# Performance work log

Measured on AMD Instinct MI355X. Metric: run time of the kernel, lower is better.

Reference implementation:

```python
import jax, jax.numpy as jnp
import numpy as np

N_NODES = 50000
N_EDGES = 800000
D_IN = 128
HIDDEN = 64
N_CLASSES = 2


def gcn_conv(x, edge_index, W, b, num_nodes):
    """PyG GCNConv: linear (no bias) -> add self-loops -> sym-normalized aggregate -> + bias."""
    h = x @ W  # [N, H]
    loop = jnp.arange(num_nodes, dtype=edge_index.dtype)
    src = jnp.concatenate([edge_index[0], loop])  # [E+N]
    dst = jnp.concatenate([edge_index[1], loop])
    deg = jax.ops.segment_sum(jnp.ones_like(dst, dtype=h.dtype), dst, num_segments=num_nodes)
    dinv = jnp.where(deg > 0, jax.lax.rsqrt(deg), 0.0)
    norm = dinv[src] * dinv[dst]  # [E+N]
    msg = h[src] * norm[:, None]  # [E+N, H]  (gather + scale)
    out = jax.ops.segment_sum(msg, dst, num_segments=num_nodes)  # scatter-add
    return out + b


def setup_inputs() -> dict:
    key = jax.random.key(0)
    ks = jax.random.split(key, 6)
    x = jax.random.normal(ks[0], (N_NODES, D_IN), dtype=jnp.float32)
    edge_index = jax.random.randint(ks[1], (2, N_EDGES), 0, N_NODES, dtype=jnp.int64)
    # Glorot-ish init for weights, zero bias (PyG default)
    W1 = jax.random.normal(ks[2], (D_IN, HIDDEN), dtype=jnp.float32) * (1.0 / np.sqrt(D_IN))
    b1 = jnp.zeros((HIDDEN,), dtype=jnp.float32)
    W2 = jax.random.normal(ks[3], (HIDDEN, N_CLASSES), dtype=jnp.float32) * (1.0 / np.sqrt(HIDDEN))
    b2 = jnp.zeros((N_CLASSES,), dtype=jnp.float32)
    return {"x": x, "edge_index": edge_index, "W1": W1, "b1": b1, "W2": W2, "b2": b2}


def reference(x, edge_index, W1, b1, W2, b2):
    h = jax.nn.relu(gcn_conv(x, edge_index, W1, b1, N_NODES))
    # F.dropout(training=self.training) is identity in eval mode
    out = gcn_conv(h, edge_index, W2, b2, N_NODES)
    return out
```

## Files before the change

### kernel.cpp

```cpp
#include <hip/hip_runtime.h>

#define N_NODES 50000
#define N_EDGES 800000
#define D_IN 128
#define HIDDEN 64
#define N_CLASSES 2
#define NBUK 782
#define NBUK_P 784
#define NBLK 196
#define NE4 200000
#define XPAD 136
#define CAP 2048

typedef _Float16 half4v __attribute__((ext_vector_type(4)));
typedef _Float16 h8 __attribute__((ext_vector_type(8)));
typedef float f4 __attribute__((ext_vector_type(4)));
typedef float f8 __attribute__((ext_vector_type(8)));


__global__ __launch_bounds__(256) void k_gemm_bin(
    const int4* __restrict__ src4, const int4* __restrict__ dst4,
    int* __restrict__ cnt, int* __restrict__ ebin,
    const float* __restrict__ x, const float* __restrict__ W1,
    _Float16* __restrict__ hs)
{
    __shared__ __attribute__((aligned(16))) _Float16 smem[2 * 64 * XPAD];
    const int t = threadIdx.x;

    if (blockIdx.x < NBLK) {
        int* hist = (int*)smem;
        int* curb = (int*)smem + NBUK_P;
        for (int i = t; i < NBUK; i += 256) hist[i] = 0;
        __syncthreads();
        int base4 = blockIdx.x * 1024;
#pragma unroll
        for (int k = 0; k < 4; k++) {
            int idx = base4 + k * 256 + t;
            if (idx < NE4) {
                int4 d = dst4[idx];
                atomicAdd(&hist[d.x >> 6], 1);
                atomicAdd(&hist[d.y >> 6], 1);
                atomicAdd(&hist[d.z >> 6], 1);
                atomicAdd(&hist[d.w >> 6], 1);
            }
        }
        __syncthreads();
        for (int i = t; i < NBUK; i += 256) {
            int c = hist[i];
            curb[i] = c ? atomicAdd(&cnt[i], c) : 0;
        }
        __syncthreads();
#pragma unroll
        for (int k = 0; k < 4; k++) {
            int idx = base4 + k * 256 + t;
            if (idx < NE4) {
                int4 sv = src4[idx];
                int4 d = dst4[idx];
                int p0 = atomicAdd(&curb[d.x >> 6], 1);
                int p1 = atomicAdd(&curb[d.y >> 6], 1);
                int p2 = atomicAdd(&curb[d.z >> 6], 1);
                int p3 = atomicAdd(&curb[d.w >> 6], 1);
                if (p0 < CAP) ebin[(d.x >> 6) * CAP + p0] = (sv.x << 7) | (d.x & 63);
                if (p1 < CAP) ebin[(d.y >> 6) * CAP + p1] = (sv.y << 7) | (d.y & 63);
                if (p2 < CAP) ebin[(d.z >> 6) * CAP + p2] = (sv.z << 7) | (d.z & 63);
                if (p3 < CAP) ebin[(d.w >> 6) * CAP + p3] = (sv.w << 7) | (d.w & 63);
            }
        }
        return;
    }

    _Float16* xs = smem;
    _Float16* Wt = smem + 64 * XPAD;
    const int gb = blockIdx.x - NBLK;
    const int row0 = gb * 64;

    for (int i4 = t; i4 < 64 * D_IN / 4; i4 += 256) {
        int r = i4 >> 5;
        int k4 = (i4 & 31) << 2;
        int grow = row0 + r;
        half4v hv;
        if (grow < N_NODES) {
            float4 v = *(const float4*)&x[grow * D_IN + k4];
            hv.x = (_Float16)v.x; hv.y = (_Float16)v.y;
            hv.z = (_Float16)v.z; hv.w = (_Float16)v.w;
        } else {
            hv.x = hv.y = hv.z = hv.w = (_Float16)0.f;
        }
        *(half4v*)&xs[r * XPAD + k4] = hv;
    }
    for (int i4 = t; i4 < D_IN * HIDDEN / 4; i4 += 256) {
        float4 v = *(const float4*)&W1[i4 * 4];
        int k = i4 >> 4;
        int n = (i4 & 15) << 2;
        Wt[(n + 0) * XPAD + k] = (_Float16)v.x;
        Wt[(n + 1) * XPAD + k] = (_Float16)v.y;
        Wt[(n + 2) * XPAD + k] = (_Float16)v.z;
        Wt[(n + 3) * XPAD + k] = (_Float16)v.w;
    }
    __syncthreads();

    const int w = t >> 6;
    const int L = t & 63;
    const int mrow = w * 16 + (L & 15);
    const int qk = (L >> 4) * 8;
    f4 acc0 = {0.f, 0.f, 0.f, 0.f}, acc1 = acc0, acc2 = acc0, acc3 = acc0;
#pragma unroll
    for (int ks = 0; ks < D_IN; ks += 32) {
        h8 a  = *(const h8*)&xs[mrow * XPAD + ks + qk];
        h8 b0 = *(const h8*)&Wt[(0 * 16 + (L & 15)) * XPAD + ks + qk];
        h8 b1 = *(const h8*)&Wt[(1 * 16 + (L & 15)) * XPAD + ks + qk];
        h8 b2 = *(const h8*)&Wt[(2 * 16 + (L & 15)) * XPAD + ks + qk];
        h8 b3 = *(const h8*)&Wt[(3 * 16 + (L & 15)) * XPAD + ks + qk];
        acc0 = __builtin_amdgcn_mfma_f32_16x16x32_f16(a, b0, acc0, 0, 0, 0);
        acc1 = __builtin_amdgcn_mfma_f32_16x16x32_f16(a, b1, acc1, 0, 0, 0);
        acc2 = __builtin_amdgcn_mfma_f32_16x16x32_f16(a, b2, acc2, 0, 0, 0);
        acc3 = __builtin_amdgcn_mfma_f32_16x16x32_f16(a, b3, acc3, 0, 0, 0);
    }

    const int n0 = L & 15;
#pragma unroll
    for (int j = 0; j < 4; j++) {
        int m = w * 16 + (L >> 4) * 4 + j;
        size_t base = (size_t)(row0 + m) * HIDDEN;
        hs[base + 0 * 16 + n0] = (_Float16)acc0[j];
        hs[base + 1 * 16 + n0] = (_Float16)acc1[j];
        hs[base + 2 * 16 + n0] = (_Float16)acc2[j];
        hs[base + 3 * 16 + n0] = (_Float16)acc3[j];
    }
}


__global__ __launch_bounds__(256) void k_csr_scale(
    const int* __restrict__ ebin, const int* __restrict__ cnt,
    int* __restrict__ rs, int* __restrict__ re, float* __restrict__ dinv_g,
    int* __restrict__ rec, _Float16* __restrict__ hs)
{
    __shared__ int cnt64[64];
    __shared__ int cur[64];
    __shared__ float sdinv[64];
    const int b = blockIdx.x;
    const int t = threadIdx.x;
    const int row0 = b * 64;
    const int beg = b * CAP;
    const int end = beg + cnt[b];

    if (t < 64) cnt64[t] = 0;
    __syncthreads();
    for (int i = beg + t; i < end; i += 256) atomicAdd(&cnt64[ebin[i] & 63], 1);
    __syncthreads();
    if (t < 64) {
        int deg = cnt64[t];
        int sum = deg;
#pragma unroll
        for (int off = 1; off < 64; off <<= 1) {
            int v = __shfl_up(sum, off, 64);
            if (t >= off) sum += v;
        }
        int ex = sum - deg;
        cur[t] = ex;
        float di = rsqrtf((float)(deg + 1));
        sdinv[t] = di;
        int node = row0 + t;
        rs[node] = beg + ex;
        re[node] = beg + ex + deg;
        dinv_g[node] = di;
    }
    __syncthreads();
    for (int i = beg + t; i < end; i += 256) {
        int pk = ebin[i];
        int pos = atomicAdd(&cur[pk & 63], 1);
        rec[beg + pos] = pk >> 7;
    }
    for (int i = t; i < 64 * HIDDEN / 8; i += 256) {
        int r = i >> 3;
        int c = (i & 7) << 3;
        size_t base = (size_t)(row0 + r) * HIDDEN + c;
        h8 hv = *(const h8*)&hs[base];
        float di = sdinv[r];
#pragma unroll
        for (int k = 0; k < 8; k++) hv[k] = (_Float16)((float)hv[k] * di);
        *(h8*)&hs[base] = hv;
    }
}


__global__ __launch_bounds__(256) void k_agg1_l2(
    const _Float16* __restrict__ hs, const int* __restrict__ rs,
    const int* __restrict__ re,
    const int* __restrict__ rec, const float* __restrict__ dinv,
    const float* __restrict__ b1, const float* __restrict__ W2,
    float* __restrict__ zs)
{
    const int node = blockIdx.x * 32 + (threadIdx.x >> 3);
    const int g = threadIdx.x & 7;
    const int gbase = threadIdx.x & 56;
    const h8* H = (const h8*)hs;

    float di = dinv[node];
    f8 acc = {};

    int beg = rs[node];
    int end = re[node];

    for (int base = beg; base < end; base += 16) {
        int n = end - base;
        if (n > 16) n = 16;
        int r0 = (2 * g     < n) ? rec[base + 2 * g]     : N_NODES;
        int r1 = (2 * g + 1 < n) ? rec[base + 2 * g + 1] : N_NODES;
        int n8 = (n + 7) & ~7;
        for (int e = 0; e < n8; e += 8) {
            int q = gbase + (e >> 1);
            int s0 = __shfl(r0, q + 0, 64);
            int s1 = __shfl(r1, q + 0, 64);
            int s2 = __shfl(r0, q + 1, 64);
            int s3 = __shfl(r1, q + 1, 64);
            int s4 = __shfl(r0, q + 2, 64);
            int s5 = __shfl(r1, q + 2, 64);
            int s6 = __shfl(r0, q + 3, 64);
            int s7 = __shfl(r1, q + 3, 64);
            h8 a0 = H[s0 * 8 + g];
            h8 a1 = H[s1 * 8 + g];
            h8 a2 = H[s2 * 8 + g];
            h8 a3 = H[s3 * 8 + g];
            h8 a4 = H[s4 * 8 + g];
            h8 a5 = H[s5 * 8 + g];
            h8 a6 = H[s6 * 8 + g];
            h8 a7 = H[s7 * 8 + g];
#pragma unroll
            for (int k = 0; k < 8; k++) {
                acc[k] += (((float)a0[k] + (float)a1[k]) + ((float)a2[k] + (float)a3[k]))
                        + (((float)a4[k] + (float)a5[k]) + ((float)a6[k] + (float)a7[k]));
            }
        }
    }

    h8 sv = H[node * 8 + g];
#pragma unroll
    for (int k = 0; k < 8; k++) acc[k] += (float)sv[k];

    float4 bbA = ((const float4*)b1)[2 * g];
    float4 bbB = ((const float4*)b1)[2 * g + 1];
    float y[8];
    y[0] = fmaxf(fmaf(acc[0], di, bbA.x), 0.f);
    y[1] = fmaxf(fmaf(acc[1], di, bbA.y), 0.f);
    y[2] = fmaxf(fmaf(acc[2], di, bbA.z), 0.f);
    y[3] = fmaxf(fmaf(acc[3], di, bbA.w), 0.f);
    y[4] = fmaxf(fmaf(acc[4], di, bbB.x), 0.f);
    y[5] = fmaxf(fmaf(acc[5], di, bbB.y), 0.f);
    y[6] = fmaxf(fmaf(acc[6], di, bbB.z), 0.f);
    y[7] = fmaxf(fmaf(acc[7], di, bbB.w), 0.f);
    float p0 = 0.f, p1 = 0.f;
    const float4* W2f4 = (const float4*)W2;
#pragma unroll
    for (int m = 0; m < 4; m++) {
        float4 q = W2f4[4 * g + m];
        p0 += y[2 * m] * q.x + y[2 * m + 1] * q.z;
        p1 += y[2 * m] * q.y + y[2 * m + 1] * q.w;
    }

    p0 += __shfl_down(p0, 4, 64);
    p1 += __shfl_down(p1, 4, 64);
    p0 += __shfl_down(p0, 2, 64);
    p1 += __shfl_down(p1, 2, 64);
    p0 += __shfl_down(p0, 1, 64);
    p1 += __shfl_down(p1, 1, 64);
    if (g == 0) {
        zs[node * 2 + 0] = p0 * di;
        zs[node * 2 + 1] = p1 * di;
    }
}


__global__ __launch_bounds__(256) void k_agg2(
    const float* __restrict__ zs, const int* __restrict__ rs,
    const int* __restrict__ re,
    const int* __restrict__ rec, const float* __restrict__ dinv,
    const float* __restrict__ b2, float* __restrict__ out)
{
    const int node = blockIdx.x * 32 + (threadIdx.x >> 3);
    const int j = threadIdx.x & 7;
    if (node >= N_NODES) return;
    int beg = rs[node];
    int end = re[node];
    float a0 = 0.f, a1 = 0.f;
    for (int idx = beg + j; idx < end; idx += 8) {
        int s = rec[idx];
        float2 v = *(const float2*)&zs[s * 2];
        a0 += v.x;
        a1 += v.y;
    }
    a0 += __shfl_down(a0, 4, 64);
    a1 += __shfl_down(a1, 4, 64);
    a0 += __shfl_down(a0, 2, 64);
    a1 += __shfl_down(a1, 2, 64);
    a0 += __shfl_down(a0, 1, 64);
    a1 += __shfl_down(a1, 1, 64);
    if (j == 0) {
        float di = dinv[node];
        float2 zv = *(const float2*)&zs[node * 2];
        float2 o;
        o.x = fmaf(di, a0 + zv.x, b2[0]);
        o.y = fmaf(di, a1 + zv.y, b2[1]);
        *(float2*)&out[node * 2] = o;
    }
}


extern "C" void kernel_launch(void* const* d_in, const int* in_sizes, int n_in,
                              void* d_out, int out_size, void* d_ws, size_t ws_size,
                              hipStream_t stream) {
    const float* x  = (const float*)d_in[0];
    const int* ei   = (const int*)d_in[1];
    const float* W1 = (const float*)d_in[2];
    const float* b1 = (const float*)d_in[3];
    const float* W2 = (const float*)d_in[4];
    const float* b2 = (const float*)d_in[5];
    float* out = (float*)d_out;

    const int4* src4 = (const int4*)ei;
    const int4* dst4 = (const int4*)(ei + N_EDGES);

    int*      cnt  = (int*)d_ws;
    float*    dinv = (float*)d_ws + 2048;
    int*      rs   = (int*)d_ws + 53248;
    int*      re   = (int*)d_ws + 104448;
    int*      ebin = (int*)d_ws + 155648;
    int*      rec  = (int*)d_ws + 1757184;
    _Float16* hs   = (_Float16*)((int*)d_ws + 3358720);
    float*    zs   = (float*)d_ws + 4960256;

    hipMemsetAsync(cnt, 0, 1024 * sizeof(int), stream);
    k_gemm_bin<<<NBLK + NBUK, 256, 0, stream>>>(src4, dst4, cnt, ebin, x, W1, hs);
    k_csr_scale<<<NBUK, 256, 0, stream>>>(ebin, cnt, rs, re, dinv, rec, hs);
    k_agg1_l2<<<(N_NODES + 31) / 32, 256, 0, stream>>>(hs, rs, re, rec, dinv, b1, W2, zs);
    k_agg2<<<(N_NODES + 31) / 32, 256, 0, stream>>>(zs, rs, re, rec, dinv, b2, out);
}
```

Measured before the change: 120.2 us.

## Prefetch edge indices in aggregation loops and cache edge bins in registers/LDS

New measurement: 122.8 us. 1.02x slower.

```diff
diff --git a/kernel.cpp b/kernel.cpp
--- a/kernel.cpp
+++ b/kernel.cpp
@@ -6,7 +6,6 @@
 #define HIDDEN 64
 #define N_CLASSES 2
 #define NBUK 782
-#define NBUK_P 784
 #define NBLK 196
 #define NE4 200000
 #define XPAD 136
@@ -29,41 +28,43 @@
 
     if (blockIdx.x < NBLK) {
         int* hist = (int*)smem;
-        int* curb = (int*)smem + NBUK_P;
         for (int i = t; i < NBUK; i += 256) hist[i] = 0;
         __syncthreads();
         int base4 = blockIdx.x * 1024;
+        int4 dv[4], sv[4];
+        bool val[4];
 #pragma unroll
         for (int k = 0; k < 4; k++) {
             int idx = base4 + k * 256 + t;
-            if (idx < NE4) {
-                int4 d = dst4[idx];
-                atomicAdd(&hist[d.x >> 6], 1);
-                atomicAdd(&hist[d.y >> 6], 1);
-                atomicAdd(&hist[d.z >> 6], 1);
-                atomicAdd(&hist[d.w >> 6], 1);
+            val[k] = (idx < NE4);
+            if (val[k]) {
+                dv[k] = dst4[idx];
+                sv[k] = src4[idx];
+                atomicAdd(&hist[dv[k].x >> 6], 1);
+                atomicAdd(&hist[dv[k].y >> 6], 1);
+                atomicAdd(&hist[dv[k].z >> 6], 1);
+                atomicAdd(&hist[dv[k].w >> 6], 1);
             }
         }
         __syncthreads();
         for (int i = t; i < NBUK; i += 256) {
             int c = hist[i];
-            curb[i] = c ? atomicAdd(&cnt[i], c) : 0;
+            hist[i] = c ? atomicAdd(&cnt[i], c) : 0;
         }
         __syncthreads();
 #pragma unroll
         for (int k = 0; k < 4; k++) {
-            int idx = base4 + k * 256 + t;
-            if (idx < NE4) {
-                int4 sv = src4[idx];
-                int4 d = dst4[idx];
-                int p0 = atomicAdd(&curb[d.x >> 6], 1);
-                int p1 = atomicAdd(&curb[d.y >> 6], 1);
-                int p2 = atomicAdd(&curb[d.z >> 6], 1);
-                int p3 = atomicAdd(&curb[d.w >> 6], 1);
-                if (p0 < CAP) ebin[(d.x >> 6) * CAP + p0] = (sv.x << 7) | (d.x & 63);
-                if (p1 < CAP) ebin[(d.y >> 6) * CAP + p1] = (sv.y << 7) | (d.y & 63);
-                if (p2 < CAP) ebin[(d.z >> 6) * CAP + p2] = (sv.z << 7) | (d.z & 63);
-                if (p3 < CAP) ebin[(d.w >> 6) * CAP + p3] = (sv.w << 7) | (d.w & 63);
+            if (val[k]) {
+                int b0 = dv[k].x >> 6, b1 = dv[k].y >> 6;
+                int b2 = dv[k].z >> 6, b3 = dv[k].w >> 6;
+                int p0 = atomicAdd(&hist[b0], 1);
+                int p1 = atomicAdd(&hist[b1], 1);
+                int p2 = atomicAdd(&hist[b2], 1);
+                int p3 = atomicAdd(&hist[b3], 1);
+                if (p0 < CAP) ebin[b0 * CAP + p0] = (sv[k].x << 7) | (dv[k].x & 63);
+                if (p1 < CAP) ebin[b1 * CAP + p1] = (sv[k].y << 7) | (dv[k].y & 63);
+                if (p2 < CAP) ebin[b2 * CAP + p2] = (sv[k].z << 7) | (dv[k].z & 63);
+                if (p3 < CAP) ebin[b3 * CAP + p3] = (sv[k].w << 7) | (dv[k].w & 63);
             }
         }
         return;
@@ -135,6 +136,7 @@
     int* __restrict__ rs, int* __restrict__ re, float* __restrict__ dinv_g,
     int* __restrict__ rec, _Float16* __restrict__ hs)
 {
+    __shared__ int lbin[CAP];
     __shared__ int cnt64[64];
     __shared__ int cur[64];
     __shared__ float sdinv[64];
@@ -142,11 +144,15 @@
     const int t = threadIdx.x;
     const int row0 = b * 64;
     const int beg = b * CAP;
-    const int end = beg + cnt[b];
+    const int m = cnt[b];
 
     if (t < 64) cnt64[t] = 0;
     __syncthreads();
-    for (int i = beg + t; i < end; i += 256) atomicAdd(&cnt64[ebin[i] & 63], 1);
+    for (int i = t; i < m; i += 256) {
+        int pk = ebin[beg + i];
+        lbin[i] = pk;
+        atomicAdd(&cnt64[pk & 63], 1);
+    }
     __syncthreads();
     if (t < 64) {
         int deg = cnt64[t];
@@ -166,8 +172,8 @@
         dinv_g[node] = di;
     }
     __syncthreads();
-    for (int i = beg + t; i < end; i += 256) {
-        int pk = ebin[i];
+    for (int i = t; i < m; i += 256) {
+        int pk = lbin[i];
         int pos = atomicAdd(&cur[pk & 63], 1);
         rec[beg + pos] = pk >> 7;
     }
@@ -202,11 +208,23 @@
     int beg = rs[node];
     int end = re[node];
 
+    int r0 = N_NODES, r1 = N_NODES;
+    if (beg < end) {
+        int n0 = end - beg; if (n0 > 16) n0 = 16;
+        if (2 * g     < n0) r0 = rec[beg + 2 * g];
+        if (2 * g + 1 < n0) r1 = rec[beg + 2 * g + 1];
+    }
+
     for (int base = beg; base < end; base += 16) {
+        int nb = base + 16;
+        int nr0 = N_NODES, nr1 = N_NODES;
+        if (nb < end) {
+            int nn = end - nb; if (nn > 16) nn = 16;
+            if (2 * g     < nn) nr0 = rec[nb + 2 * g];
+            if (2 * g + 1 < nn) nr1 = rec[nb + 2 * g + 1];
+        }
         int n = end - base;
         if (n > 16) n = 16;
-        int r0 = (2 * g     < n) ? rec[base + 2 * g]     : N_NODES;
-        int r1 = (2 * g + 1 < n) ? rec[base + 2 * g + 1] : N_NODES;
         int n8 = (n + 7) & ~7;
         for (int e = 0; e < n8; e += 8) {
             int q = gbase + (e >> 1);
@@ -232,6 +250,7 @@
                         + (((float)a4[k] + (float)a5[k]) + ((float)a6[k] + (float)a7[k]));
             }
         }
+        r0 = nr0; r1 = nr1;
     }
 
     h8 sv = H[node * 8 + g];
@@ -283,11 +302,16 @@
     int beg = rs[node];
     int end = re[node];
     float a0 = 0.f, a1 = 0.f;
-    for (int idx = beg + j; idx < end; idx += 8) {
-        int s = rec[idx];
+    int idx = beg + j;
+    int s = (idx < end) ? rec[idx] : 0;
+    while (idx < end) {
+        int nidx = idx + 8;
+        int ns = (nidx < end) ? rec[nidx] : 0;
         float2 v = *(const float2*)&zs[s * 2];
         a0 += v.x;
         a1 += v.y;
+        idx = nidx;
+        s = ns;
     }
     a0 += __shfl_down(a0, 4, 64);
     a1 += __shfl_down(a1, 4, 64);
```

## Split hidden features into two halves and aggregate each half in separate passes

Applied to the files above, without the earlier changes.

New measurement: 129.1 us. 7.4% more time.

```diff
diff --git a/kernel.cpp b/kernel.cpp
--- a/kernel.cpp
+++ b/kernel.cpp
@@ -15,14 +15,13 @@
 typedef _Float16 half4v __attribute__((ext_vector_type(4)));
 typedef _Float16 h8 __attribute__((ext_vector_type(8)));
 typedef float f4 __attribute__((ext_vector_type(4)));
-typedef float f8 __attribute__((ext_vector_type(8)));
 
 
 __global__ __launch_bounds__(256) void k_gemm_bin(
     const int4* __restrict__ src4, const int4* __restrict__ dst4,
     int* __restrict__ cnt, int* __restrict__ ebin,
     const float* __restrict__ x, const float* __restrict__ W1,
-    _Float16* __restrict__ hs)
+    _Float16* __restrict__ hs0, _Float16* __restrict__ hs1)
 {
     __shared__ __attribute__((aligned(16))) _Float16 smem[2 * 64 * XPAD];
     const int t = threadIdx.x;
@@ -121,11 +120,11 @@
 #pragma unroll
     for (int j = 0; j < 4; j++) {
         int m = w * 16 + (L >> 4) * 4 + j;
-        size_t base = (size_t)(row0 + m) * HIDDEN;
-        hs[base + 0 * 16 + n0] = (_Float16)acc0[j];
-        hs[base + 1 * 16 + n0] = (_Float16)acc1[j];
-        hs[base + 2 * 16 + n0] = (_Float16)acc2[j];
-        hs[base + 3 * 16 + n0] = (_Float16)acc3[j];
+        size_t bh = (size_t)(row0 + m) * 32;
+        hs0[bh + n0]      = (_Float16)acc0[j];
+        hs0[bh + 16 + n0] = (_Float16)acc1[j];
+        hs1[bh + n0]      = (_Float16)acc2[j];
+        hs1[bh + 16 + n0] = (_Float16)acc3[j];
     }
 }
 
@@ -133,7 +132,7 @@
 __global__ __launch_bounds__(256) void k_csr_scale(
     const int* __restrict__ ebin, const int* __restrict__ cnt,
     int* __restrict__ rs, int* __restrict__ re, float* __restrict__ dinv_g,
-    int* __restrict__ rec, _Float16* __restrict__ hs)
+    int* __restrict__ rec, _Float16* __restrict__ hs0, _Float16* __restrict__ hs1)
 {
     __shared__ int cnt64[64];
     __shared__ int cur[64];
@@ -171,33 +170,35 @@
         int pos = atomicAdd(&cur[pk & 63], 1);
         rec[beg + pos] = pk >> 7;
     }
-    for (int i = t; i < 64 * HIDDEN / 8; i += 256) {
-        int r = i >> 3;
-        int c = (i & 7) << 3;
-        size_t base = (size_t)(row0 + r) * HIDDEN + c;
-        h8 hv = *(const h8*)&hs[base];
+    for (int i = t; i < 512; i += 256) {
+        int sel = i >> 8;
+        int idx = i & 255;
+        int r = idx >> 2;
+        int c = (idx & 3) << 3;
+        _Float16* hp = sel ? hs1 : hs0;
+        size_t base = (size_t)(row0 + r) * 32 + c;
+        h8 hv = *(const h8*)&hp[base];
         float di = sdinv[r];
 #pragma unroll
         for (int k = 0; k < 8; k++) hv[k] = (_Float16)((float)hv[k] * di);
-        *(h8*)&hs[base] = hv;
-    }
-}
-
-
-__global__ __launch_bounds__(256) void k_agg1_l2(
-    const _Float16* __restrict__ hs, const int* __restrict__ rs,
-    const int* __restrict__ re,
-    const int* __restrict__ rec, const float* __restrict__ dinv,
-    const float* __restrict__ b1, const float* __restrict__ W2,
-    float* __restrict__ zs)
+        *(h8*)&hp[base] = hv;
+    }
+}
+
+
+__global__ __launch_bounds__(256) void k_agg1_half(
+    const _Float16* __restrict__ hsh, const int* __restrict__ rs,
+    const int* __restrict__ re, const int* __restrict__ rec,
+    const float* __restrict__ dinv, const float* __restrict__ b1h,
+    const float* __restrict__ W2h, float* __restrict__ zs, int accum)
 {
     const int node = blockIdx.x * 32 + (threadIdx.x >> 3);
     const int g = threadIdx.x & 7;
     const int gbase = threadIdx.x & 56;
-    const h8* H = (const h8*)hs;
+    const half4v* H = (const half4v*)hsh;
 
     float di = dinv[node];
-    f8 acc = {};
+    f4 acc = {0.f, 0.f, 0.f, 0.f};
 
     int beg = rs[node];
     int end = re[node];
@@ -218,45 +219,40 @@
             int s5 = __shfl(r1, q + 2, 64);
             int s6 = __shfl(r0, q + 3, 64);
             int s7 = __shfl(r1, q + 3, 64);
-            h8 a0 = H[s0 * 8 + g];
-            h8 a1 = H[s1 * 8 + g];
-            h8 a2 = H[s2 * 8 + g];
-            h8 a3 = H[s3 * 8 + g];
-            h8 a4 = H[s4 * 8 + g];
-            h8 a5 = H[s5 * 8 + g];
-            h8 a6 = H[s6 * 8 + g];
-            h8 a7 = H[s7 * 8 + g];
-#pragma unroll
-            for (int k = 0; k < 8; k++) {
-                acc[k] += (((float)a0[k] + (float)a1[k]) + ((float)a2[k] + (float)a3[k]))
-                        + (((float)a4[k] + (float)a5[k]) + ((float)a6[k] + (float)a7[k]));
-            }
-        }
-    }
-
-    h8 sv = H[node * 8 + g];
-#pragma unroll
-    for (int k = 0; k < 8; k++) acc[k] += (float)sv[k];
-
-    float4 bbA = ((const float4*)b1)[2 * g];
-    float4 bbB = ((const float4*)b1)[2 * g + 1];
-    float y[8];
-    y[0] = fmaxf(fmaf(acc[0], di, bbA.x), 0.f);
-    y[1] = fmaxf(fmaf(acc[1], di, bbA.y), 0.f);
-    y[2] = fmaxf(fmaf(acc[2], di, bbA.z), 0.f);
-    y[3] = fmaxf(fmaf(acc[3], di, bbA.w), 0.f);
-    y[4] = fmaxf(fmaf(acc[4], di, bbB.x), 0.f);
-    y[5] = fmaxf(fmaf(acc[5], di, bbB.y), 0.f);
-    y[6] = fmaxf(fmaf(acc[6], di, bbB.z), 0.f);
-    y[7] = fmaxf(fmaf(acc[7], di, bbB.w), 0.f);
-    float p0 = 0.f, p1 = 0.f;
-    const float4* W2f4 = (const float4*)W2;
-#pragma unroll
-    for (int m = 0; m < 4; m++) {
-        float4 q = W2f4[4 * g + m];
-        p0 += y[2 * m] * q.x + y[2 * m + 1] * q.z;
-        p1 += y[2 * m] * q.y + y[2 * m + 1] * q.w;
-    }
+            half4v a0 = H[s0 * 8 + g];
+            half4v a1 = H[s1 * 8 + g];
+            half4v a2 = H[s2 * 8 + g];
+            half4v a3 = H[s3 * 8 + g];
+            half4v a4 = H[s4 * 8 + g];
+            half4v a5 = H[s5 * 8 + g];
+            half4v a6 = H[s6 * 8 + g];
+            half4v a7 = H[s7 * 8 + g];
+            acc.x += (((float)a0.x + (float)a1.x) + ((float)a2.x + (float)a3.x))
+                   + (((float)a4.x + (float)a5.x) + ((float)a6.x + (float)a7.x));
+            acc.y += (((float)a0.y + (float)a1.y) + ((float)a2.y + (float)a3.y))
+                   + (((float)a4.y + (float)a5.y) + ((float)a6.y + (float)a7.y));
+            acc.z += (((float)a0.z + (float)a1.z) + ((float)a2.z + (float)a3.z))
+                   + (((float)a4.z + (float)a5.z) + ((float)a6.z + (float)a7.z));
+            acc.w += (((float)a0.w + (float)a1.w) + ((float)a2.w + (float)a3.w))
+                   + (((float)a4.w + (float)a5.w) + ((float)a6.w + (float)a7.w));
+        }
+    }
+
+    half4v sv = H[node * 8 + g];
+    acc.x += (float)sv.x;
+    acc.y += (float)sv.y;
+    acc.z += (float)sv.z;
+    acc.w += (float)sv.w;
+
+    float4 bb = ((const float4*)b1h)[g];
+    float y0 = fmaxf(fmaf(acc.x, di, bb.x), 0.f);
+    float y1 = fmaxf(fmaf(acc.y, di, bb.y), 0.f);
+    float y2 = fmaxf(fmaf(acc.z, di, bb.z), 0.f);
+    float y3 = fmaxf(fmaf(acc.w, di, bb.w), 0.f);
+    float4 qA = ((const float4*)W2h)[2 * g];
+    float4 qB = ((const float4*)W2h)[2 * g + 1];
+    float p0 = y0 * qA.x + y1 * qA.z + y2 * qB.x + y3 * qB.z;
+    float p1 = y0 * qA.y + y1 * qA.w + y2 * qB.y + y3 * qB.w;
 
     p0 += __shfl_down(p0, 4, 64);
     p1 += __shfl_down(p1, 4, 64);
@@ -265,8 +261,15 @@
     p0 += __shfl_down(p0, 1, 64);
     p1 += __shfl_down(p1, 1, 64);
     if (g == 0) {
-        zs[node * 2 + 0] = p0 * di;
-        zs[node * 2 + 1] = p1 * di;
+        float v0 = p0 * di;
+        float v1 = p1 * di;
+        if (accum) {
+            zs[node * 2 + 0] += v0;
+            zs[node * 2 + 1] += v1;
+        } else {
+            zs[node * 2 + 0] = v0;
+            zs[node * 2 + 1] = v1;
+        }
     }
 }
 
@@ -326,12 +329,14 @@
     int*      re   = (int*)d_ws + 104448;
     int*      ebin = (int*)d_ws + 155648;
     int*      rec  = (int*)d_ws + 1757184;
-    _Float16* hs   = (_Float16*)((int*)d_ws + 3358720);
+    _Float16* hs0  = (_Float16*)((int*)d_ws + 3358720);
+    _Float16* hs1  = (_Float16*)((int*)d_ws + 4159488);
     float*    zs   = (float*)d_ws + 4960256;
 
     hipMemsetAsync(cnt, 0, 1024 * sizeof(int), stream);
-    k_gemm_bin<<<NBLK + NBUK, 256, 0, stream>>>(src4, dst4, cnt, ebin, x, W1, hs);
-    k_csr_scale<<<NBUK, 256, 0, stream>>>(ebin, cnt, rs, re, dinv, rec, hs);
-    k_agg1_l2<<<(N_NODES + 31) / 32, 256, 0, stream>>>(hs, rs, re, rec, dinv, b1, W2, zs);
+    k_gemm_bin<<<NBLK + NBUK, 256, 0, stream>>>(src4, dst4, cnt, ebin, x, W1, hs0, hs1);
+    k_csr_scale<<<NBUK, 256, 0, stream>>>(ebin, cnt, rs, re, dinv, rec, hs0, hs1);
+    k_agg1_half<<<(N_NODES + 31) / 32, 256, 0, stream>>>(hs0, rs, re, rec, dinv, b1, W2, zs, 0);
+    k_agg1_half<<<(N_NODES + 31) / 32, 256, 0, stream>>>(hs1, rs, re, rec, dinv, b1 + 32, W2 + 64, zs, 1);
     k_agg2<<<(N_NODES + 31) / 32, 256, 0, stream>>>(zs, rs, re, rec, dinv, b2, out);
 }
```
